# Performance work log

Measured on AMD Instinct MI355X. Metric: run time of the kernel, lower is better.

Reference implementation:

```python
import jax, jax.numpy as jnp
import numpy as np

N = 4096
D_FEAT = 64


def setup_inputs() -> dict:
    key = jax.random.key(0)
    kx, ky = jax.random.split(key)
    xINP = jax.random.normal(kx, (N, D_FEAT), dtype=jnp.float32)
    yINP = jax.random.normal(ky, (N, D_FEAT), dtype=jnp.float32)
    return {"xINP": xINP, "yINP": yINP}


def _greedy_match(xINP, yINP):
    n = xINP.shape[0]
    # Euclidean (p=2) distance matrix, same as scipy.spatial.distance_matrix
    x2 = jnp.sum(xINP * xINP, axis=1)[:, None]           # [n, 1]
    y2 = jnp.sum(yINP * yINP, axis=1)[None, :]           # [1, n]
    sq = jnp.maximum(x2 + y2 - 2.0 * (xINP @ yINP.T), 0.0)
    cost = jnp.sqrt(sq)                                   # [n, n]
    # sorted() with key is stable; jnp.argsort is stable by default
    order = jnp.argsort(cost.reshape(-1))                 # [n*n]

    row0 = jnp.full((n,), -1, dtype=jnp.int32)
    col0 = jnp.full((n,), -1, dtype=jnp.int32)

    def body(k, state):
        row, col = state
        idx = order[k]
        i = idx // n
        j = idx % n
        free = (row[i] == -1) & (col[j] == -1)
        row = row.at[i].set(jnp.where(free, j.astype(jnp.int32), row[i]))
        col = col.at[j].set(jnp.where(free, i.astype(jnp.int32), col[j]))
        return (row, col)

    row, _col = jax.lax.fori_loop(0, n * n, body, (row0, col0))
    return row  # row_to_col_match_vec, int32 in [-1, n)


def reference(xINP, yINP):
    return _greedy_match(xINP, yINP)
```

## Files before the change

kernel.cpp:

```cpp
#include <hip/hip_runtime.h>

#define N 4096
#define D 64
#define TCAP 1024
#define TTHRESH 96
#define SNB 256
#define SNT 512
#define S0B 1024
#define S0T 512
#define RPAIRS 9

typedef unsigned long long u64;
#define LO32(k) ((int)(unsigned)((k) & 0xffffffffull))

__device__ float g_C[(size_t)N * (size_t)N];
__device__ float g_tailC[(size_t)TCAP * TCAP];
__device__ float4 g_yT[N * 16];
__device__ float g_x2[N], g_y2[N];
__device__ int   g_rowMatch[N];
__device__ int   g_freeRows[2][N];
__device__ int   g_freeCols[2][N];
__device__ u64   g_rowMinR[2][N];
__device__ u64   g_rowMin2[2][N];
__device__ u64   g_colMin[2][N];
__device__ u64   g_colMin2[2][N];
__device__ int   g_nr[2], g_nc[2];
__device__ int   g_done, g_finalCur;

__device__ inline u64 shfl_down_u64(u64 v, int d) {
  unsigned lo = (unsigned)(v & 0xffffffffull);
  unsigned hi = (unsigned)(v >> 32);
  lo = __shfl_down(lo, d, 64);
  hi = __shfl_down(hi, d, 64);
  return ((u64)hi << 32) | (u64)lo;
}

__device__ inline void block_rowmin_reduce8(u64* best, int rows, u64* s_part) {
  const int tid = threadIdx.x;
  const int lane = tid & 63;
  const int wv = tid >> 6;
#pragma unroll
  for (int r = 0; r < 16; ++r) {
    if (r < rows) {
      u64 v = best[r];
#pragma unroll
      for (int d = 32; d > 0; d >>= 1) {
        u64 o = shfl_down_u64(v, d);
        v = (o < v) ? o : v;
      }
      if (lane == 0) s_part[r * 8 + wv] = v;
    }
  }
  __syncthreads();
  if (tid < rows) {
    u64 mn = s_part[tid * 8];
#pragma unroll
    for (int w = 1; w < 8; ++w) {
      u64 o = s_part[tid * 8 + w];
      mn = (o < mn) ? o : mn;
    }
    s_part[128 + tid] = mn;
  }
}

__device__ __forceinline__ float f4e(const float4* a, int e) {
  float4 v = a[e >> 2];
  switch (e & 3) {
    case 0: return v.x;
    case 1: return v.y;
    case 2: return v.z;
    default: return v.w;
  }
}

__device__ __forceinline__ void insert2(u64* m1, u64* m2, u64 k) {
  if (k == ~0ull) return;
  u64 old = atomicMin((unsigned long long*)m1, k);
  u64 loser = (k < old) ? old : k;
  if (loser != ~0ull) atomicMin((unsigned long long*)m2, loser);
}

__global__ void __launch_bounds__(256) k_init(const float* __restrict__ x,
                                              const float* __restrict__ y) {
  const int i = blockIdx.x * 256 + threadIdx.x;
  const float4* xr4 = reinterpret_cast<const float4*>(x + (size_t)i * D);
  const float4* yr4 = reinterpret_cast<const float4*>(y + (size_t)i * D);

  {
    float4 xv[16];
#pragma unroll
    for (int k = 0; k < 16; ++k) xv[k] = xr4[k];
    float qx[8];
#pragma unroll
    for (int j = 0; j < 8; ++j) {
      float v = f4e(xv, j);
      qx[j] = __fmul_rn(v, v);
    }
#pragma unroll
    for (int m = 8; m < D; m += 8) {
#pragma unroll
      for (int j = 0; j < 8; ++j) {
        float v = f4e(xv, m + j);
        qx[j] = __fadd_rn(qx[j], __fmul_rn(v, v));
      }
    }
    g_x2[i] = __fadd_rn(__fadd_rn(__fadd_rn(qx[0], qx[1]), __fadd_rn(qx[2], qx[3])),
                        __fadd_rn(__fadd_rn(qx[4], qx[5]), __fadd_rn(qx[6], qx[7])));
  }
  {
    float4 yv[16];
#pragma unroll
    for (int k = 0; k < 16; ++k) yv[k] = yr4[k];
    float qy[8];
#pragma unroll
    for (int j = 0; j < 8; ++j) {
      float w = f4e(yv, j);
      qy[j] = __fmul_rn(w, w);
    }
#pragma unroll
    for (int m = 8; m < D; m += 8) {
#pragma unroll
      for (int j = 0; j < 8; ++j) {
        float w = f4e(yv, m + j);
        qy[j] = __fadd_rn(qy[j], __fmul_rn(w, w));
      }
    }
    g_y2[i] = __fadd_rn(__fadd_rn(__fadd_rn(qy[0], qy[1]), __fadd_rn(qy[2], qy[3])),
                        __fadd_rn(__fadd_rn(qy[4], qy[5]), __fadd_rn(qy[6], qy[7])));
#pragma unroll
    for (int k = 0; k < 16; ++k) g_yT[(k << 12) + i] = yv[k];
  }

  g_rowMatch[i] = -1;
  g_freeRows[0][i] = i;
  g_freeCols[0][i] = i;
  g_rowMinR[0][i] = ~0ull;
  g_rowMinR[1][i] = ~0ull;
  g_rowMin2[0][i] = ~0ull;
  g_rowMin2[1][i] = ~0ull;
  g_colMin[0][i] = ~0ull;
  g_colMin[1][i] = ~0ull;
  g_colMin2[0][i] = ~0ull;
  g_colMin2[1][i] = ~0ull;
  if (i == 0) {
    g_nr[0] = N; g_nc[0] = N; g_nr[1] = 0; g_nc[1] = 0;
    g_done = 0;
    g_finalCur = ((RPAIRS & 1) ^ 1);
  }
}

__global__ void __launch_bounds__(S0T) k_scan0(const float* __restrict__ x,
                                               const float* __restrict__ y) {
  __shared__ u64 s_part[64 + 8];
  const int tid = threadIdx.x;
  const int r0 = (blockIdx.x >> 1) << 3;
  const int h = blockIdx.x & 1;

  float x2r[8];
#pragma unroll
  for (int r = 0; r < 8; ++r) x2r[r] = g_x2[r0 + r];
  u64 best[8];
#pragma unroll
  for (int r = 0; r < 8; ++r) best[r] = ~0ull;

  const int c0 = tid + (h << 11);
  float acc[8][4];
#pragma unroll
  for (int r = 0; r < 8; ++r)
#pragma unroll
    for (int k = 0; k < 4; ++k) acc[r][k] = 0.0f;

#pragma unroll
  for (int kc = 0; kc < 16; ++kc) {
    const float4* ytk = g_yT + (kc << 12);
    float4 yv0 = ytk[c0];
    float4 yv1 = ytk[c0 + 512];
    float4 yv2 = ytk[c0 + 1024];
    float4 yv3 = ytk[c0 + 1536];
#pragma unroll
    for (int r = 0; r < 8; ++r) {
      float4 xv = reinterpret_cast<const float4*>(x + (size_t)(r0 + r) * D)[kc];
      acc[r][0] = fmaf(xv.x, yv0.x, acc[r][0]);
      acc[r][0] = fmaf(xv.y, yv0.y, acc[r][0]);
      acc[r][0] = fmaf(xv.z, yv0.z, acc[r][0]);
      acc[r][0] = fmaf(xv.w, yv0.w, acc[r][0]);
      acc[r][1] = fmaf(xv.x, yv1.x, acc[r][1]);
      acc[r][1] = fmaf(xv.y, yv1.y, acc[r][1]);
      acc[r][1] = fmaf(xv.z, yv1.z, acc[r][1]);
      acc[r][1] = fmaf(xv.w, yv1.w, acc[r][1]);
      acc[r][2] = fmaf(xv.x, yv2.x, acc[r][2]);
      acc[r][2] = fmaf(xv.y, yv2.y, acc[r][2]);
      acc[r][2] = fmaf(xv.z, yv2.z, acc[r][2]);
      acc[r][2] = fmaf(xv.w, yv2.w, acc[r][2]);
      acc[r][3] = fmaf(xv.x, yv3.x, acc[r][3]);
      acc[r][3] = fmaf(xv.y, yv3.y, acc[r][3]);
      acc[r][3] = fmaf(xv.z, yv3.z, acc[r][3]);
      acc[r][3] = fmaf(xv.w, yv3.w, acc[r][3]);
    }
  }

#pragma unroll
  for (int k = 0; k < 4; ++k) {
    const int c = c0 + (k << 9);
    const float y2j = g_y2[c];
    u64 ckey = ~0ull;
#pragma unroll
    for (int r = 0; r < 8; ++r) {
      float t = __fadd_rn(x2r[r], y2j);
      float sq = __fsub_rn(t, __fmul_rn(2.0f, acc[r][k]));
      sq = fmaxf(sq, 0.0f);
      float cost = __fsqrt_rn(sq);
      g_C[(size_t)(r0 + r) * N + c] = cost;
      u64 cb = ((u64)__float_as_uint(cost)) << 32;
      u64 rk = cb | (unsigned)c;
      best[r] = (rk < best[r]) ? rk : best[r];
      u64 ck = cb | (unsigned)(r0 + r);
      ckey = (ck < ckey) ? ck : ckey;
    }
    u64 curv = g_colMin[0][c];
    if (ckey < curv) atomicMin((unsigned long long*)&g_colMin[0][c], ckey);
  }

  {
    const int lane = tid & 63, wv = tid >> 6;
#pragma unroll
    for (int r = 0; r < 8; ++r) {
      u64 v = best[r];
#pragma unroll
      for (int d = 32; d > 0; d >>= 1) {
        u64 o = shfl_down_u64(v, d);
        v = (o < v) ? o : v;
      }
      if (lane == 0) s_part[r * 8 + wv] = v;
    }
    __syncthreads();
    if (tid < 8) {
      u64 mn = s_part[tid * 8];
#pragma unroll
      for (int w = 1; w < 8; ++w) {
        u64 o = s_part[tid * 8 + w];
        mn = (o < mn) ? o : mn;
      }
      u64 curv = g_rowMinR[0][r0 + tid];
      if (mn < curv) atomicMin((unsigned long long*)&g_rowMinR[0][r0 + tid], mn);
    }
  }
  (void)y;
}

__global__ void __launch_bounds__(SNT, 2) k_scanN(int round) {
  if (g_done) return;
  const int cur = round & 1;
  const int nr = g_nr[cur], nc = g_nc[cur];
  const int tid = threadIdx.x, bid = blockIdx.x;

  for (int t = bid * SNT + tid; t < N; t += SNB * SNT) {
    g_colMin[cur ^ 1][t] = ~0ull;
    g_colMin2[cur ^ 1][t] = ~0ull;
    g_rowMinR[cur ^ 1][t] = ~0ull;
    g_rowMin2[cur ^ 1][t] = ~0ull;
  }

  const int ngroups = (nr + 15) >> 4;
  int lgS = 0;
  while (lgS < 4 && (ngroups << (lgS + 1)) <= SNB) ++lgS;
  const int S = 1 << lgS;
  if (bid >= (ngroups << lgS)) return;
  const int g = bid >> lgS;
  const int s = bid & (S - 1);

  __shared__ u64 s_cp1[4096];
  __shared__ u64 s_cp2[4096];
  __shared__ u64 s_p1[128 + 16];
  __shared__ u64 s_p2[128 + 16];
  __shared__ int s_irow[16];

  const int r0 = g << 4;
  const int rows = min(16, nr - r0);
  if (tid < 16) {
    int rr = (tid < rows) ? (r0 + tid) : r0;
    s_irow[tid] = g_freeRows[cur][rr];
  }
  const int cstart = (s << 9) + tid;
  const int cstep = S << 9;
  for (int c = cstart; c < nc; c += cstep) { s_cp1[c] = ~0ull; s_cp2[c] = ~0ull; }
  __syncthreads();

  int ir[16];
#pragma unroll
  for (int r = 0; r < 16; ++r) ir[r] = s_irow[r];
  u64 b1[16], b2[16];
#pragma unroll
  for (int r = 0; r < 16; ++r) { b1[r] = ~0ull; b2[r] = ~0ull; }

  for (int c = cstart; c < nc; c += cstep) {
    const int j = g_freeCols[cur][c];
    u64 c1 = s_cp1[c], c2 = s_cp2[c];
#pragma unroll
    for (int r = 0; r < 16; ++r) {
      if (r < rows) {
        float cost = g_C[(size_t)ir[r] * N + j];
        u64 cb = ((u64)__float_as_uint(cost)) << 32;
        u64 rk = cb | (unsigned)j;
        if (rk < b1[r]) { b2[r] = b1[r]; b1[r] = rk; }
        else if (rk < b2[r]) b2[r] = rk;
        u64 ck = cb | (unsigned)ir[r];
        if (ck < c1) { c2 = c1; c1 = ck; }
        else if (ck < c2) c2 = ck;
      }
    }
    s_cp1[c] = c1; s_cp2[c] = c2;
  }

  {
    const int lane = tid & 63, wv = tid >> 6;
#pragma unroll
    for (int r = 0; r < 16; ++r) {
      if (r < rows) {
        u64 v1 = b1[r], v2 = b2[r];
#pragma unroll
        for (int d = 32; d > 0; d >>= 1) {
          u64 o1 = shfl_down_u64(v1, d);
          u64 o2 = shfl_down_u64(v2, d);
          u64 n1 = (v1 < o1) ? v1 : o1;
          u64 hi = (v1 < o1) ? o1 : v1;
          u64 lo = (v2 < o2) ? v2 : o2;
          v1 = n1;
          v2 = (hi < lo) ? hi : lo;
        }
        if (lane == 0) { s_p1[r * 8 + wv] = v1; s_p2[r * 8 + wv] = v2; }
      }
    }
    __syncthreads();
    if (tid < rows) {
      u64 m1 = s_p1[tid * 8], m2 = s_p2[tid * 8];
#pragma unroll
      for (int w = 1; w < 8; ++w) {
        u64 o1 = s_p1[tid * 8 + w], o2 = s_p2[tid * 8 + w];
        u64 n1 = (m1 < o1) ? m1 : o1;
        u64 hi = (m1 < o1) ? o1 : m1;
        u64 lo = (m2 < o2) ? m2 : o2;
        m1 = n1;
        m2 = (hi < lo) ? hi : lo;
      }
      const int i = s_irow[tid];
      insert2(&g_rowMinR[cur][i], &g_rowMin2[cur][i], m1);
      insert2(&g_rowMinR[cur][i], &g_rowMin2[cur][i], m2);
    }
  }

  for (int c = cstart; c < nc; c += cstep) {
    u64 k1 = s_cp1[c];
    if (k1 != ~0ull) {
      const int j = g_freeCols[cur][c];
      insert2(&g_colMin[cur][j], &g_colMin2[cur][j], k1);
      insert2(&g_colMin[cur][j], &g_colMin2[cur][j], s_cp2[c]);
    }
  }
}

__global__ void __launch_bounds__(SNT) k_match(int round) {
  if (g_done) return;
  const int cur = round & 1, nxt = cur ^ 1;
  const int tid = threadIdx.x, bid = blockIdx.x;
  const int nr = g_nr[cur], nc = g_nc[cur];
  __shared__ int s_wc[8];
  __shared__ int s_base;

  const int lane = tid & 63, wv = tid >> 6;
  if (bid == 0) {
    if (tid == 0) s_base = 0;
    __syncthreads();
    for (int start = 0; start < nr; start += SNT) {
      int r = start + tid;
      int keep = 0; int iv = -1;
      if (r < nr) {
        int i = g_freeRows[cur][r];
        iv = i;
        u64 rm1 = g_rowMinR[cur][i];
        int j1 = LO32(rm1);
        int i1 = LO32(g_colMin[cur][j1]);
        if (i1 == i) {
          g_rowMatch[i] = j1;
        } else {
          int jc = -1;
          bool j1gone = (LO32(g_rowMinR[cur][i1]) == j1);
          if (!j1gone) jc = j1;
          else {
            u64 rm2 = g_rowMin2[cur][i];
            if (rm2 != ~0ull) {
              int j2 = LO32(rm2);
              int i2 = LO32(g_colMin[cur][j2]);
              if (LO32(g_rowMinR[cur][i2]) != j2) jc = j2;
            }
          }
          int rc = -1;
          if (jc >= 0) {
            int r1 = LO32(g_colMin[cur][jc]);
            int jr1 = LO32(g_rowMinR[cur][r1]);
            bool r1m = (LO32(g_colMin[cur][jr1]) == r1);
            if (!r1m) rc = r1;
            else {
              u64 cm2 = g_colMin2[cur][jc];
              if (cm2 != ~0ull) {
                int r2 = LO32(cm2);
                int jr2 = LO32(g_rowMinR[cur][r2]);
                if (LO32(g_colMin[cur][jr2]) != r2) rc = r2;
              }
            }
          }
          if (jc >= 0 && rc == i) g_rowMatch[i] = jc;
          else keep = 1;
        }
      }
      u64 bm = __ballot(keep);
      int pre = __popcll(bm & ((1ull << lane) - 1ull));
      if (lane == 0) s_wc[wv] = __popcll(bm);
      __syncthreads();
      int off = 0, tot = 0;
#pragma unroll
      for (int w = 0; w < 8; ++w) { off += (w < wv) ? s_wc[w] : 0; tot += s_wc[w]; }
      if (keep) g_freeRows[nxt][s_base + off + pre] = iv;
      __syncthreads();
      if (tid == 0) s_base += tot;
      __syncthreads();
    }
    if (tid == 0) {
      int nnr = s_base;
      g_nr[nxt] = nnr;
      if (nnr <= TTHRESH || nnr >= nr) { g_finalCur = nxt; g_done = 1; }
    }
  } else {
    if (tid == 0) s_base = 0;
    __syncthreads();
    for (int start = 0; start < nc; start += SNT) {
      int c = start + tid;
      int keep = 0; int jv = -1;
      if (c < nc) {
        int j = g_freeCols[cur][c];
        jv = j;
        u64 cm1 = g_colMin[cur][j];
        int i1 = LO32(cm1);
        if (LO32(g_rowMinR[cur][i1]) == j) {
        } else {
          int rc = -1;
          {
            int r1 = i1;
            int jr1 = LO32(g_rowMinR[cur][r1]);
            bool r1m = (LO32(g_colMin[cur][jr1]) == r1);
            if (!r1m) rc = r1;
            else {
              u64 cm2 = g_colMin2[cur][j];
              if (cm2 != ~0ull) {
                int r2 = LO32(cm2);
                int jr2 = LO32(g_rowMinR[cur][r2]);
                if (LO32(g_colMin[cur][jr2]) != r2) rc = r2;
              }
            }
          }
          int jc = -1;
          if (rc >= 0) {
            int jA = LO32(g_rowMinR[cur][rc]);
            int iA = LO32(g_colMin[cur][jA]);
            bool jAgone = (LO32(g_rowMinR[cur][iA]) == jA);
            if (!jAgone) jc = jA;
            else {
              u64 rm2 = g_rowMin2[cur][rc];
              if (rm2 != ~0ull) {
                int jB = LO32(rm2);
                int iB = LO32(g_colMin[cur][jB]);
                if (LO32(g_rowMinR[cur][iB]) != jB) jc = jB;
              }
            }
          }
          if (!(rc >= 0 && jc == j)) keep = 1;
        }
      }
      u64 bm = __ballot(keep);
      int pre = __popcll(bm & ((1ull << lane) - 1ull));
      if (lane == 0) s_wc[wv] = __popcll(bm);
      __syncthreads();
      int off = 0, tot = 0;
#pragma unroll
      for (int w = 0; w < 8; ++w) { off += (w < wv) ? s_wc[w] : 0; tot += s_wc[w]; }
      if (keep) g_freeCols[nxt][s_base + off + pre] = jv;
      __syncthreads();
      if (tid == 0) s_base += tot;
      __syncthreads();
    }
    if (tid == 0) g_nc[nxt] = s_base;
  }
}

__global__ void __launch_bounds__(SNT) k_gather() {
  const int fc = g_finalCur;
  const int mr = g_nr[fc], mc = g_nc[fc];
  if (mr <= 0 || mr > TCAP || mc <= 0 || mc > TCAP) return;
  const int tid = threadIdx.x, bid = blockIdx.x;
  for (int rr = bid; rr < mr; rr += SNB) {
    const int irow = g_freeRows[fc][rr];
    const float* src = g_C + (size_t)irow * N;
    float* dst = g_tailC + (size_t)rr * TCAP;
    for (int c = tid; c < mc; c += SNT) {
      dst[c] = src[g_freeCols[fc][c]];
    }
  }
}

__global__ void __launch_bounds__(1024, 1) k_tail(int* __restrict__ out) {
  __shared__ int s_rpos[2][TCAP], s_cpos[2][TCAP];
  __shared__ int s_rbest[TCAP];
  __shared__ u64 s_cmin[TCAP];
  __shared__ int s_wc[16];
  const int tid = threadIdx.x;
  const int lane = tid & 63, wv = tid >> 6;

  const int fc = g_finalCur;
  int mr = g_nr[fc], mc = g_nc[fc];
  if (mr < 0 || mr > TCAP || mc < 0 || mc > TCAP) mr = 0;
  for (int t = tid; t < mr; t += 1024) s_rpos[0][t] = t;
  for (int t = tid; t < mc; t += 1024) s_cpos[0][t] = t;
  __syncthreads();

  int tcur = 0;
  for (int round = 0; round < 2048 && mr > 0; ++round) {
    const int nit = (mc + 63) >> 6;
    int cpv[16];
#pragma unroll
    for (int k = 0; k < 16; ++k) {
      int ci = (k << 6) + lane;
      cpv[k] = (k < nit && ci < mc) ? s_cpos[tcur][ci] : 0;
    }
    for (int rr = wv; rr < mr; rr += 16) {
      const int rp = s_rpos[tcur][rr];
      const float* rowp = g_tailC + (size_t)rp * TCAP;
      u64 best = ~0ull;
#pragma unroll
      for (int k = 0; k < 16; ++k) {
        if (k < nit) {
          int ci = (k << 6) + lane;
          if (ci < mc) {
            float cost = rowp[cpv[k]];
            u64 key = (((u64)__float_as_uint(cost)) << 32) | (unsigned)ci;
            best = (key < best) ? key : best;
          }
        }
      }
#pragma unroll
      for (int d = 32; d > 0; d >>= 1) {
        u64 o = shfl_down_u64(best, d);
        best = (o < best) ? o : best;
      }
      if (lane == 0) s_rbest[rr] = (int)(best & 0xffffffffull);
    }
    __syncthreads();
    if (tid < mc) {
      const int cp = s_cpos[tcur][tid];
      const float* colp = g_tailC + cp;
      u64 best = ~0ull;
      int r = 0;
      for (; r + 4 <= mr; r += 4) {
#pragma unroll
        for (int q = 0; q < 4; ++q) {
          int rp = s_rpos[tcur][r + q];
          float cost = colp[(size_t)rp * TCAP];
          u64 key = (((u64)__float_as_uint(cost)) << 32) | (unsigned)(r + q);
          best = (key < best) ? key : best;
        }
      }
      for (; r < mr; ++r) {
        int rp = s_rpos[tcur][r];
        float cost = colp[(size_t)rp * TCAP];
        u64 key = (((u64)__float_as_uint(cost)) << 32) | (unsigned)r;
        best = (key < best) ? key : best;
      }
      s_cmin[tid] = best;
    }
    __syncthreads();
    int keep = 0;
    if (tid < mr) {
      int q = s_rbest[tid];
      if ((int)(unsigned)(s_cmin[q] & 0xffffffffull) == tid) {
        g_rowMatch[g_freeRows[fc][s_rpos[tcur][tid]]] = g_freeCols[fc][s_cpos[tcur][q]];
      } else keep = 1;
    }
    u64 bm = __ballot(keep);
    int pre = __popcll(bm & ((1ull << lane) - 1ull));
    if (lane == 0) s_wc[wv] = __popcll(bm);
    __syncthreads();
    int off = 0, tot = 0;
#pragma unroll
    for (int w = 0; w < 16; ++w) { off += (w < wv) ? s_wc[w] : 0; tot += s_wc[w]; }
    if (keep) s_rpos[tcur ^ 1][off + pre] = s_rpos[tcur][tid];
    int newmr = tot;
    __syncthreads();
    int keepc = 0;
    if (tid < mc) {
      int r2 = (int)(unsigned)(s_cmin[tid] & 0xffffffffull);
      if (s_rbest[r2] != tid) keepc = 1;
    }
    u64 bm2 = __ballot(keepc);
    int pre2 = __popcll(bm2 & ((1ull << lane) - 1ull));
    if (lane == 0) s_wc[wv] = __popcll(bm2);
    __syncthreads();
    int off2 = 0, tot2 = 0;
#pragma unroll
    for (int w = 0; w < 16; ++w) { off2 += (w < wv) ? s_wc[w] : 0; tot2 += s_wc[w]; }
    if (keepc) s_cpos[tcur ^ 1][off2 + pre2] = s_cpos[tcur][tid];
    __syncthreads();
    if (newmr >= mr) break;
    mr = newmr; mc = tot2; tcur ^= 1;
  }
  __syncthreads();
  for (int i = tid; i < N; i += 1024) out[i] = g_rowMatch[i];
}

extern "C" void kernel_launch(void* const* d_in, const int* in_sizes, int n_in,
                              void* d_out, int out_size, void* d_ws, size_t ws_size,
                              hipStream_t stream) {
  const float* x = (const float*)d_in[0];
  const float* y = (const float*)d_in[1];
  int* out = (int*)d_out;
  k_init<<<16, 256, 0, stream>>>(x, y);
  k_scan0<<<S0B, S0T, 0, stream>>>(x, y);
  k_match<<<2, SNT, 0, stream>>>(0);
  for (int r = 1; r <= RPAIRS; ++r) {
    k_scanN<<<SNB, SNT, 0, stream>>>(r);
    k_match<<<2, SNT, 0, stream>>>(r);
  }
  k_gather<<<SNB, SNT, 0, stream>>>();
  k_tail<<<1, 1024, 0, stream>>>(out);
  (void)in_sizes; (void)n_in; (void)out_size; (void)d_ws; (void)ws_size;
}
```

Before: 709.1 us.

## Parallelize match/compaction kernel across many blocks with atomic-append free lists

The match kernel used to run on two blocks, each looping serially over all free rows or columns with block-wide prefix sums. It now launches 256 blocks, one element per thread, and compacts the surviving indices with a wave ballot plus one atomicAdd per wave onto global counters. The counters are reset at the start of each scan round. The early-termination flag (g_done/TTHRESH) is removed, so all rounds always run and the final buffer index is fixed. The free-list order becomes nondeterministic, and rounds that used to be skipped after convergence may now add work.

```diff
diff --git a/kernel.cpp b/kernel.cpp
--- a/kernel.cpp
+++ b/kernel.cpp
@@ -3,7 +3,6 @@
 #define N 4096
 #define D 64
 #define TCAP 1024
-#define TTHRESH 96
 #define SNB 256
 #define SNT 512
 #define S0B 1024
@@ -25,7 +24,7 @@
 __device__ u64   g_colMin[2][N];
 __device__ u64   g_colMin2[2][N];
 __device__ int   g_nr[2], g_nc[2];
-__device__ int   g_done, g_finalCur;
+__device__ int   g_finalCur;
 
 __device__ inline u64 shfl_down_u64(u64 v, int d) {
   unsigned lo = (unsigned)(v & 0xffffffffull);
@@ -33,34 +32,6 @@
   lo = __shfl_down(lo, d, 64);
   hi = __shfl_down(hi, d, 64);
   return ((u64)hi << 32) | (u64)lo;
-}
-
-__device__ inline void block_rowmin_reduce8(u64* best, int rows, u64* s_part) {
-  const int tid = threadIdx.x;
-  const int lane = tid & 63;
-  const int wv = tid >> 6;
-#pragma unroll
-  for (int r = 0; r < 16; ++r) {
-    if (r < rows) {
-      u64 v = best[r];
-#pragma unroll
-      for (int d = 32; d > 0; d >>= 1) {
-        u64 o = shfl_down_u64(v, d);
-        v = (o < v) ? o : v;
-      }
-      if (lane == 0) s_part[r * 8 + wv] = v;
-    }
-  }
-  __syncthreads();
-  if (tid < rows) {
-    u64 mn = s_part[tid * 8];
-#pragma unroll
-    for (int w = 1; w < 8; ++w) {
-      u64 o = s_part[tid * 8 + w];
-      mn = (o < mn) ? o : mn;
-    }
-    s_part[128 + tid] = mn;
-  }
 }
 
 __device__ __forceinline__ float f4e(const float4* a, int e) {
@@ -144,7 +115,6 @@
   g_colMin2[1][i] = ~0ull;
   if (i == 0) {
     g_nr[0] = N; g_nc[0] = N; g_nr[1] = 0; g_nc[1] = 0;
-    g_done = 0;
     g_finalCur = ((RPAIRS & 1) ^ 1);
   }
 }
@@ -249,11 +219,11 @@
 }
 
 __global__ void __launch_bounds__(SNT, 2) k_scanN(int round) {
-  if (g_done) return;
   const int cur = round & 1;
   const int nr = g_nr[cur], nc = g_nc[cur];
   const int tid = threadIdx.x, bid = blockIdx.x;
 
+  if (bid == 0 && tid == 0) { g_nr[cur ^ 1] = 0; g_nc[cur ^ 1] = 0; }
   for (int t = bid * SNT + tid; t < N; t += SNB * SNT) {
     g_colMin[cur ^ 1][t] = ~0ull;
     g_colMin2[cur ^ 1][t] = ~0ull;
@@ -360,135 +330,111 @@
 }
 
 __global__ void __launch_bounds__(SNT) k_match(int round) {
-  if (g_done) return;
   const int cur = round & 1, nxt = cur ^ 1;
   const int tid = threadIdx.x, bid = blockIdx.x;
-  const int nr = g_nr[cur], nc = g_nc[cur];
-  __shared__ int s_wc[8];
-  __shared__ int s_base;
-
-  const int lane = tid & 63, wv = tid >> 6;
-  if (bid == 0) {
-    if (tid == 0) s_base = 0;
-    __syncthreads();
-    for (int start = 0; start < nr; start += SNT) {
-      int r = start + tid;
-      int keep = 0; int iv = -1;
-      if (r < nr) {
-        int i = g_freeRows[cur][r];
-        iv = i;
-        u64 rm1 = g_rowMinR[cur][i];
-        int j1 = LO32(rm1);
-        int i1 = LO32(g_colMin[cur][j1]);
-        if (i1 == i) {
-          g_rowMatch[i] = j1;
-        } else {
-          int jc = -1;
-          bool j1gone = (LO32(g_rowMinR[cur][i1]) == j1);
-          if (!j1gone) jc = j1;
+  const int lane = tid & 63;
+
+  if (bid < 128) {
+    const int nr = g_nr[cur];
+    int r = bid * SNT + tid;
+    int keep = 0; int iv = -1;
+    if (r < nr) {
+      int i = g_freeRows[cur][r];
+      iv = i;
+      u64 rm1 = g_rowMinR[cur][i];
+      int j1 = LO32(rm1);
+      int i1 = LO32(g_colMin[cur][j1]);
+      if (i1 == i) {
+        g_rowMatch[i] = j1;
+      } else {
+        int jc = -1;
+        bool j1gone = (LO32(g_rowMinR[cur][i1]) == j1);
+        if (!j1gone) jc = j1;
+        else {
+          u64 rm2 = g_rowMin2[cur][i];
+          if (rm2 != ~0ull) {
+            int j2 = LO32(rm2);
+            int i2 = LO32(g_colMin[cur][j2]);
+            if (LO32(g_rowMinR[cur][i2]) != j2) jc = j2;
+          }
+        }
+        int rc = -1;
+        if (jc >= 0) {
+          int r1 = LO32(g_colMin[cur][jc]);
+          int jr1 = LO32(g_rowMinR[cur][r1]);
+          bool r1m = (LO32(g_colMin[cur][jr1]) == r1);
+          if (!r1m) rc = r1;
           else {
-            u64 rm2 = g_rowMin2[cur][i];
-            if (rm2 != ~0ull) {
-              int j2 = LO32(rm2);
-              int i2 = LO32(g_colMin[cur][j2]);
-              if (LO32(g_rowMinR[cur][i2]) != j2) jc = j2;
+            u64 cm2 = g_colMin2[cur][jc];
+            if (cm2 != ~0ull) {
+              int r2 = LO32(cm2);
+              int jr2 = LO32(g_rowMinR[cur][r2]);
+              if (LO32(g_colMin[cur][jr2]) != r2) rc = r2;
             }
           }
-          int rc = -1;
-          if (jc >= 0) {
-            int r1 = LO32(g_colMin[cur][jc]);
-            int jr1 = LO32(g_rowMinR[cur][r1]);
-            bool r1m = (LO32(g_colMin[cur][jr1]) == r1);
-            if (!r1m) rc = r1;
-            else {
-              u64 cm2 = g_colMin2[cur][jc];
-              if (cm2 != ~0ull) {
-                int r2 = LO32(cm2);
-                int jr2 = LO32(g_rowMinR[cur][r2]);
-                if (LO32(g_colMin[cur][jr2]) != r2) rc = r2;
-              }
+        }
+        if (jc >= 0 && rc == i) g_rowMatch[i] = jc;
+        else keep = 1;
+      }
+    }
+    u64 bm = __ballot(keep);
+    int pre = __popcll(bm & ((1ull << lane) - 1ull));
+    int cnt = __popcll(bm);
+    int base = 0;
+    if (lane == 0 && cnt) base = atomicAdd(&g_nr[nxt], cnt);
+    base = __shfl(base, 0, 64);
+    if (keep) g_freeRows[nxt][base + pre] = iv;
+  } else {
+    const int nc = g_nc[cur];
+    int c = (bid - 128) * SNT + tid;
+    int keep = 0; int jv = -1;
+    if (c < nc) {
+      int j = g_freeCols[cur][c];
+      jv = j;
+      u64 cm1 = g_colMin[cur][j];
+      int i1 = LO32(cm1);
+      if (LO32(g_rowMinR[cur][i1]) == j) {
+      } else {
+        int rc = -1;
+        {
+          int r1 = i1;
+          int jr1 = LO32(g_rowMinR[cur][r1]);
+          bool r1m = (LO32(g_colMin[cur][jr1]) == r1);
+          if (!r1m) rc = r1;
+          else {
+            u64 cm2 = g_colMin2[cur][j];
+            if (cm2 != ~0ull) {
+              int r2 = LO32(cm2);
+              int jr2 = LO32(g_rowMinR[cur][r2]);
+              if (LO32(g_colMin[cur][jr2]) != r2) rc = r2;
             }
           }
-          if (jc >= 0 && rc == i) g_rowMatch[i] = jc;
-          else keep = 1;
-        }
-      }
-      u64 bm = __ballot(keep);
-      int pre = __popcll(bm & ((1ull << lane) - 1ull));
-      if (lane == 0) s_wc[wv] = __popcll(bm);
-      __syncthreads();
-      int off = 0, tot = 0;
-#pragma unroll
-      for (int w = 0; w < 8; ++w) { off += (w < wv) ? s_wc[w] : 0; tot += s_wc[w]; }
-      if (keep) g_freeRows[nxt][s_base + off + pre] = iv;
-      __syncthreads();
-      if (tid == 0) s_base += tot;
-      __syncthreads();
-    }
-    if (tid == 0) {
-      int nnr = s_base;
-      g_nr[nxt] = nnr;
-      if (nnr <= TTHRESH || nnr >= nr) { g_finalCur = nxt; g_done = 1; }
-    }
-  } else {
-    if (tid == 0) s_base = 0;
-    __syncthreads();
-    for (int start = 0; start < nc; start += SNT) {
-      int c = start + tid;
-      int keep = 0; int jv = -1;
-      if (c < nc) {
-        int j = g_freeCols[cur][c];
-        jv = j;
-        u64 cm1 = g_colMin[cur][j];
-        int i1 = LO32(cm1);
-        if (LO32(g_rowMinR[cur][i1]) == j) {
-        } else {
-          int rc = -1;
-          {
-            int r1 = i1;
-            int jr1 = LO32(g_rowMinR[cur][r1]);
-            bool r1m = (LO32(g_colMin[cur][jr1]) == r1);
-            if (!r1m) rc = r1;
-            else {
-              u64 cm2 = g_colMin2[cur][j];
-              if (cm2 != ~0ull) {
-                int r2 = LO32(cm2);
-                int jr2 = LO32(g_rowMinR[cur][r2]);
-                if (LO32(g_colMin[cur][jr2]) != r2) rc = r2;
-              }
+        }
+        int jc = -1;
+        if (rc >= 0) {
+          int jA = LO32(g_rowMinR[cur][rc]);
+          int iA = LO32(g_colMin[cur][jA]);
+          bool jAgone = (LO32(g_rowMinR[cur][iA]) == jA);
+          if (!jAgone) jc = jA;
+          else {
+            u64 rm2 = g_rowMin2[cur][rc];
+            if (rm2 != ~0ull) {
+              int jB = LO32(rm2);
+              int iB = LO32(g_colMin[cur][jB]);
+              if (LO32(g_rowMinR[cur][iB]) != jB) jc = jB;
             }
           }
-          int jc = -1;
-          if (rc >= 0) {
-            int jA = LO32(g_rowMinR[cur][rc]);
-            int iA = LO32(g_colMin[cur][jA]);
-            bool jAgone = (LO32(g_rowMinR[cur][iA]) == jA);
-            if (!jAgone) jc = jA;
-            else {
-              u64 rm2 = g_rowMin2[cur][rc];
-              if (rm2 != ~0ull) {
-                int jB = LO32(rm2);
-                int iB = LO32(g_colMin[cur][jB]);
-                if (LO32(g_rowMinR[cur][iB]) != jB) jc = jB;
-              }
-            }
-          }
-          if (!(rc >= 0 && jc == j)) keep = 1;
-        }
-      }
-      u64 bm = __ballot(keep);
-      int pre = __popcll(bm & ((1ull << lane) - 1ull));
-      if (lane == 0) s_wc[wv] = __popcll(bm);
-      __syncthreads();
-      int off = 0, tot = 0;
-#pragma unroll
-      for (int w = 0; w < 8; ++w) { off += (w < wv) ? s_wc[w] : 0; tot += s_wc[w]; }
-      if (keep) g_freeCols[nxt][s_base + off + pre] = jv;
-      __syncthreads();
-      if (tid == 0) s_base += tot;
-      __syncthreads();
-    }
-    if (tid == 0) g_nc[nxt] = s_base;
+        }
+        if (!(rc >= 0 && jc == j)) keep = 1;
+      }
+    }
+    u64 bm = __ballot(keep);
+    int pre = __popcll(bm & ((1ull << lane) - 1ull));
+    int cnt = __popcll(bm);
+    int base = 0;
+    if (lane == 0 && cnt) base = atomicAdd(&g_nc[nxt], cnt);
+    base = __shfl(base, 0, 64);
+    if (keep) g_freeCols[nxt][base + pre] = jv;
   }
 }
 
@@ -623,10 +569,10 @@
   int* out = (int*)d_out;
   k_init<<<16, 256, 0, stream>>>(x, y);
   k_scan0<<<S0B, S0T, 0, stream>>>(x, y);
-  k_match<<<2, SNT, 0, stream>>>(0);
+  k_match<<<SNB, SNT, 0, stream>>>(0);
   for (int r = 1; r <= RPAIRS; ++r) {
     k_scanN<<<SNB, SNT, 0, stream>>>(r);
-    k_match<<<2, SNT, 0, stream>>>(r);
+    k_match<<<SNB, SNT, 0, stream>>>(r);
   }
   k_gather<<<SNB, SNT, 0, stream>>>();
   k_tail<<<1, 1024, 0, stream>>>(out);
```

Result: faster. 661.5 us, median of 2 (-6.7%).
